# Kernel optimization log

Hardware: AMD Instinct MI355X
Metric: run time of the kernel (lower is better)

The kernel has to match this reference:

```python
import jax, jax.numpy as jnp
import numpy as np

GRID_SIZE = 5
SPLINE_ORDER = 3
HIDDEN = 128
N = 131072
K = 256          # num_cluster
EPS = 1e-8       # torch.cosine_similarity eps
N_COEF = GRID_SIZE + SPLINE_ORDER  # 8 spline basis functions per input feature


def make_grid():
    # efficient-kan grid: grid_range [-1,1], extended by spline_order on each side
    h = 2.0 / GRID_SIZE
    g = jnp.arange(-SPLINE_ORDER, GRID_SIZE + SPLINE_ORDER + 1, dtype=jnp.float32) * h - 1.0
    return jnp.tile(g[None, :], (HIDDEN, 1))  # (in, grid_size + 2*order + 1) = (128, 12)


def b_splines(x, grid):
    # x: (N, in), grid: (in, G) -> bases: (N, in, grid_size + spline_order)
    xe = x[..., None]
    bases = ((xe >= grid[:, :-1]) & (xe < grid[:, 1:])).astype(x.dtype)
    for p in range(1, SPLINE_ORDER + 1):
        left = (xe - grid[:, :-(p + 1)]) / (grid[:, p:-1] - grid[:, :-(p + 1)])
        right = (grid[:, p + 1:] - xe) / (grid[:, p + 1:] - grid[:, 1:-p])
        bases = left * bases[..., :-1] + right * bases[..., 1:]
    return bases


def kan_linear(x, grid, base_w, spline_w, scaler):
    # efficient-kan KANLinear: base path + spline path
    base = jax.nn.silu(x) @ base_w.T                       # (N, out)
    sp = b_splines(x, grid)                                # (N, in, coef)
    sw = spline_w * scaler[..., None]                      # (out, in, coef)
    return base + jnp.einsum('nic,oic->no', sp, sw)


def setup_inputs() -> dict:
    key = jax.random.key(0)
    ks = jax.random.split(key, 9)
    s = 1.0 / np.sqrt(HIDDEN)
    return {
        'x': jax.random.normal(ks[0], (N, HIDDEN), jnp.float32),
        'prototypes': jax.random.normal(ks[1], (K, HIDDEN), jnp.float32),
        'grid': make_grid(),
        'base_w1': jax.random.normal(ks[2], (HIDDEN, HIDDEN), jnp.float32) * s,
        'spline_w1': jax.random.normal(ks[3], (HIDDEN, HIDDEN, N_COEF), jnp.float32) * 0.1,
        'scaler1': jax.random.normal(ks[4], (HIDDEN, HIDDEN), jnp.float32) * s + 1.0,
        'base_w2': jax.random.normal(ks[5], (HIDDEN, HIDDEN), jnp.float32) * s,
        'spline_w2': jax.random.normal(ks[6], (HIDDEN, HIDDEN, N_COEF), jnp.float32) * 0.1,
        'scaler2': jax.random.normal(ks[7], (HIDDEN, HIDDEN), jnp.float32) * s + 1.0,
    }


def reference(x, prototypes, grid, base_w1, spline_w1, scaler1, base_w2, spline_w2, scaler2):
    # KAN([128,128,128]) = two KANLinear layers
    h = kan_linear(x, grid, base_w1, spline_w1, scaler1)
    emb = kan_linear(h, grid, base_w2, spline_w2, scaler2)     # (N, 128)
    # cosine similarity to all prototypes = normalized matmul (same math as
    # the broadcasted torch.cosine_similarity, without the (N,K,H) intermediate)
    xn = emb / jnp.maximum(jnp.linalg.norm(emb, axis=-1, keepdims=True), EPS)
    pn = prototypes / jnp.maximum(jnp.linalg.norm(prototypes, axis=-1, keepdims=True), EPS)
    sim = xn @ pn.T                                            # (N, K)
    cluster_assignments = jnp.argmax(sim, axis=1)              # (N,)
    return emb, cluster_assignments
```

## Files before the change

kernel.cpp:

```cpp
#include <hip/hip_runtime.h>
#include <math.h>

typedef unsigned short u16;
typedef _Float16 f16;
typedef __attribute__((ext_vector_type(8))) _Float16 f16x8;
typedef __attribute__((ext_vector_type(4))) float f32x4;

#define N_ROWS 131072
#define HID 128
#define WS_CH 8192
#define N_WCH 72
#define N_PCH 8

__device__ __forceinline__ void f16_split(float v, f16& hi, f16& lo) {
    f16 h = (f16)v;
    hi = h;
    lo = (f16)(v - (float)h);
}

__device__ __forceinline__ void spline8(float xv, float* a8) {
    float s  = (xv + 2.2f) * 2.5f;
    float tf = floorf(s);
    int   tt = (int)tf;
    bool valid = (tt >= 0) && (tt <= 10);
    float kt = (float)(tt - 3) * 0.4f - 1.0f;
    float u  = (xv - kt) * 2.5f;
    float u2 = u * u, u3 = u2 * u;
    float om = 1.0f - u;
    float b3 = u3 * (1.0f / 6.0f);
    float b2 = (-3.f * u3 + 3.f * u2 + 3.f * u + 1.f) * (1.0f / 6.0f);
    float b1 = (3.f * u3 - 6.f * u2 + 4.f) * (1.0f / 6.0f);
    float b0 = om * om * om * (1.0f / 6.0f);
    #pragma unroll
    for (int c = 0; c < 8; ++c) {
        int d = tt - c;
        float v = 0.f;
        v = (d == 0) ? b3 : v;
        v = (d == 1) ? b2 : v;
        v = (d == 2) ? b1 : v;
        v = (d == 3) ? b0 : v;
        a8[c] = valid ? v : 0.f;
    }
}

#define GLOAD_LDS16(g, l)                                                         \
    __builtin_amdgcn_global_load_lds(                                             \
        (const __attribute__((address_space(1))) unsigned int*)(g),               \
        (__attribute__((address_space(3))) unsigned int*)(l), 16, 0, 0)

__global__ __launch_bounds__(256)
void pack_weights(const float* __restrict__ bw1, const float* __restrict__ sw1,
                  const float* __restrict__ sc1,
                  const float* __restrict__ bw2, const float* __restrict__ sw2,
                  const float* __restrict__ sc2,
                  const float* __restrict__ protos, u16* __restrict__ ws)
{
    int gid = blockIdx.x * 256 + threadIdx.x;
    if (gid < N_WCH * 4096) {
        int l  = gid / (36 * 4096);
        int r  = gid % (36 * 4096);
        int ch = r / 4096;
        int e  = r % 4096;
        int o  = e >> 5;
        int kl = e & 31;
        const float* bw = l ? bw2 : bw1;
        const float* sw = l ? sw2 : sw1;
        const float* sc = l ? sc2 : sc1;
        float v;
        if (ch < 4) {
            v = bw[o * HID + ch * 32 + kl];
        } else {
            int i = (ch - 4) * 4 + (kl >> 3);
            v = sw[(o * HID + i) * 8 + (kl & 7)] * sc[o * HID + i];
        }
        f16 hi, lo; f16_split(v, hi, lo);
        int nt = o >> 4, n = o & 15, kq = kl >> 3, c = kl & 7;
        size_t base = (size_t)(l * 36 + ch) * WS_CH;
        size_t idx  = ((size_t)nt * 64 + kq * 16 + n) * 8 + c;
        ws[base + idx]        = __builtin_bit_cast(u16, hi);
        ws[base + 4096 + idx] = __builtin_bit_cast(u16, lo);
    } else if (gid < (N_WCH + N_PCH) * 4096) {
        int r  = gid - N_WCH * 4096;
        int hk = r / 4096;
        int e  = r % 4096;
        int pl = e >> 5;
        int kl = e & 31;
        int half = hk >> 2, kc = hk & 3;
        float v = protos[(size_t)(half * 128 + pl) * HID + kc * 32 + kl];
        f16 hi, lo; f16_split(v, hi, lo);
        int nt = pl >> 4, n = pl & 15, kq = kl >> 3, c = kl & 7;
        size_t base = (size_t)(N_WCH + hk) * WS_CH;
        size_t idx  = ((size_t)nt * 64 + kq * 16 + n) * 8 + c;
        ws[base + idx]        = __builtin_bit_cast(u16, hi);
        ws[base + 4096 + idx] = __builtin_bit_cast(u16, lo);
    }
}

__global__ __launch_bounds__(256, 3)
void kan_fused(const float* __restrict__ x, const float* __restrict__ protos,
               const u16* __restrict__ wpack,
               float* __restrict__ emb_out, float* __restrict__ assign_out)
{
    __shared__ float t[64][132];
    __shared__ u16   Bfrag[2][8][64][8];
    __shared__ float rnp[256];

    const int tid  = threadIdx.x;
    const int lane = tid & 63;
    const int w    = tid >> 6;
    const int m    = lane & 15;
    const int q    = lane >> 4;
    const int row  = w * 16 + m;
    const int brow = blockIdx.x * 64;

    {
        const float4* pr = (const float4*)(protos + (size_t)tid * HID);
        float s = 0.0f;
        #pragma unroll
        for (int j = 0; j < 32; ++j) {
            float4 v = pr[j];
            s += v.x * v.x + v.y * v.y + v.z * v.z + v.w * v.w;
        }
        rnp[tid] = 1.0f / fmaxf(sqrtf(s), 1e-8f);
    }

    {
        const int m2 = tid >> 2, kq2 = tid & 3;
        const float4* src = (const float4*)(x + (size_t)(brow + m2) * HID + kq2 * 32);
        #pragma unroll
        for (int j = 0; j < 8; ++j) {
            float4 v = src[j];
            int k = kq2 * 32 + j * 4;
            t[m2][k] = v.x; t[m2][k + 1] = v.y; t[m2][k + 2] = v.z; t[m2][k + 3] = v.w;
        }
    }
    __syncthreads();

    union { f16x8 v; f16 h[8]; } ah, al, bh, bl;
    f32x4 acc[8];

    for (int l = 0; l < 2; ++l) {
        #pragma unroll
        for (int nt = 0; nt < 8; ++nt) acc[nt] = (f32x4){0.f, 0.f, 0.f, 0.f};

        for (int ch = 0; ch < 36; ++ch) {
            float a8[8];
            if (ch < 4) {
                #pragma unroll
                for (int j = 0; j < 8; ++j) {
                    float xv = t[row][ch * 32 + q * 8 + j];
                    a8[j] = xv / (1.0f + expf(-xv));
                }
            } else {
                spline8(t[row][(ch - 4) * 4 + q], a8);
            }
            #pragma unroll
            for (int j = 0; j < 8; ++j) f16_split(a8[j], ah.h[j], al.h[j]);

            __syncthreads();
            {
                const char* gsrc = (const char*)(wpack + (size_t)(l * 36 + ch) * WS_CH);
                char* lbase = (char*)&Bfrag[0][0][0][0] + w * 4096;
                #pragma unroll
                for (int i = 0; i < 4; ++i)
                    GLOAD_LDS16(gsrc + w * 4096 + i * 1024 + (size_t)lane * 16,
                                lbase + i * 1024);
            }
            __syncthreads();

            #pragma unroll
            for (int nt = 0; nt < 8; ++nt) {
                bh.v = *(const f16x8*)Bfrag[0][nt][lane];
                bl.v = *(const f16x8*)Bfrag[1][nt][lane];
                acc[nt] = __builtin_amdgcn_mfma_f32_16x16x32_f16(ah.v, bh.v, acc[nt], 0, 0, 0);
                acc[nt] = __builtin_amdgcn_mfma_f32_16x16x32_f16(ah.v, bl.v, acc[nt], 0, 0, 0);
                acc[nt] = __builtin_amdgcn_mfma_f32_16x16x32_f16(al.v, bh.v, acc[nt], 0, 0, 0);
                acc[nt] = __builtin_amdgcn_mfma_f32_16x16x32_f16(al.v, bl.v, acc[nt], 0, 0, 0);
            }
        }

        #pragma unroll
        for (int nt = 0; nt < 8; ++nt)
            #pragma unroll
            for (int r = 0; r < 4; ++r)
                t[w * 16 + q * 4 + r][nt * 16 + m] = acc[nt][r];
        __syncthreads();
    }

    {
        const int m2 = tid >> 2, kq2 = tid & 3;
        float* dst = emb_out + (size_t)(brow + m2) * HID + kq2 * 32;
        #pragma unroll
        for (int j = 0; j < 8; ++j)
            *(float4*)(dst + j * 4) = *(const float4*)&t[m2][kq2 * 32 + j * 4];
    }

    float best[4]; int bi[4];
    #pragma unroll
    for (int r = 0; r < 4; ++r) { best[r] = -3.402823466e+38f; bi[r] = 0; }

    for (int half = 0; half < 2; ++half) {
        #pragma unroll
        for (int nt = 0; nt < 8; ++nt) acc[nt] = (f32x4){0.f, 0.f, 0.f, 0.f};

        for (int kc = 0; kc < 4; ++kc) {
            float a8[8];
            #pragma unroll
            for (int j = 0; j < 8; ++j) a8[j] = t[row][kc * 32 + q * 8 + j];
            #pragma unroll
            for (int j = 0; j < 8; ++j) f16_split(a8[j], ah.h[j], al.h[j]);

            __syncthreads();
            {
                const char* gsrc =
                    (const char*)(wpack + (size_t)(N_WCH + half * 4 + kc) * WS_CH);
                char* lbase = (char*)&Bfrag[0][0][0][0] + w * 4096;
                #pragma unroll
                for (int i = 0; i < 4; ++i)
                    GLOAD_LDS16(gsrc + w * 4096 + i * 1024 + (size_t)lane * 16,
                                lbase + i * 1024);
            }
            __syncthreads();

            #pragma unroll
            for (int nt = 0; nt < 8; ++nt) {
                bh.v = *(const f16x8*)Bfrag[0][nt][lane];
                bl.v = *(const f16x8*)Bfrag[1][nt][lane];
                acc[nt] = __builtin_amdgcn_mfma_f32_16x16x32_f16(ah.v, bh.v, acc[nt], 0, 0, 0);
                acc[nt] = __builtin_amdgcn_mfma_f32_16x16x32_f16(ah.v, bl.v, acc[nt], 0, 0, 0);
                acc[nt] = __builtin_amdgcn_mfma_f32_16x16x32_f16(al.v, bh.v, acc[nt], 0, 0, 0);
                acc[nt] = __builtin_amdgcn_mfma_f32_16x16x32_f16(al.v, bl.v, acc[nt], 0, 0, 0);
            }
        }

        #pragma unroll
        for (int nt = 0; nt < 8; ++nt) {
            int p = half * 128 + nt * 16 + m;
            float rp = rnp[p];
            #pragma unroll
            for (int r = 0; r < 4; ++r) {
                float v = acc[nt][r] * rp;
                if (v > best[r]) { best[r] = v; bi[r] = p; }
            }
        }
    }

    #pragma unroll
    for (int r = 0; r < 4; ++r) {
        #pragma unroll
        for (int off = 1; off < 16; off <<= 1) {
            float ov = __shfl_xor(best[r], off);
            int   oi = __shfl_xor(bi[r], off);
            if (ov > best[r] || (ov == best[r] && oi < bi[r])) { best[r] = ov; bi[r] = oi; }
        }
        if (m == 0)
            assign_out[(size_t)brow + w * 16 + q * 4 + r] = (float)bi[r];
    }
}

extern "C" void kernel_launch(void* const* d_in, const int* in_sizes, int n_in,
                              void* d_out, int out_size, void* d_ws, size_t ws_size,
                              hipStream_t stream) {
    (void)in_sizes; (void)n_in; (void)out_size; (void)ws_size;

    const float* x      = (const float*)d_in[0];
    const float* protos = (const float*)d_in[1];
    const float* bw1 = (const float*)d_in[3];
    const float* sw1 = (const float*)d_in[4];
    const float* sc1 = (const float*)d_in[5];
    const float* bw2 = (const float*)d_in[6];
    const float* sw2 = (const float*)d_in[7];
    const float* sc2 = (const float*)d_in[8];

    float* out    = (float*)d_out;
    float* embp   = out;
    float* assign = out + (size_t)N_ROWS * HID;
    u16*   wpack  = (u16*)d_ws;

    pack_weights<<<dim3((N_WCH + N_PCH) * 4096 / 256), dim3(256), 0, stream>>>(
        bw1, sw1, sc1, bw2, sw2, sc2, protos, wpack);
    kan_fused<<<dim3(N_ROWS / 64), dim3(256), 0, stream>>>(
        x, protos, wpack, embp, assign);
}
```

Baseline: 455.7 us.

## Register-prefetch weight chunks, drop lo*lo MFMA term, use fast SiLU

Weight loading moves from direct global-to-LDS loads to a register prefetch: the next chunk is issued into registers while the current chunk's MFMAs run, then stored to LDS after a barrier. This hides global load latency behind compute. The split-f16 product also drops the lo*lo MFMA, going from four to three per tile. SiLU now uses fast exp and rcp with vectorized LDS reads. These changes cut MFMA work and stall time at the cost of slightly lower precision and more registers held for the prefetch.

Result: faster. 425.1 us (-6.7%).

```diff
diff --git a/kernel.cpp b/kernel.cpp
--- a/kernel.cpp
+++ b/kernel.cpp
@@ -42,11 +42,6 @@
         a8[c] = valid ? v : 0.f;
     }
 }
-
-#define GLOAD_LDS16(g, l)                                                         \
-    __builtin_amdgcn_global_load_lds(                                             \
-        (const __attribute__((address_space(1))) unsigned int*)(g),               \
-        (__attribute__((address_space(3))) unsigned int*)(l), 16, 0, 0)
 
 __global__ __launch_bounds__(256)
 void pack_weights(const float* __restrict__ bw1, const float* __restrict__ sw1,
@@ -112,6 +107,27 @@
     const int q    = lane >> 4;
     const int row  = w * 16 + m;
     const int brow = blockIdx.x * 64;
+    const int woff = w * 256 + lane;
+
+    uint4 rr0, rr1, rr2, rr3;
+
+#define ISSUE_LOADS(region) do {                                                   \
+        const uint4* _g = (const uint4*)(wpack + (size_t)(region) * WS_CH) + woff; \
+        rr0 = _g[0]; rr1 = _g[64]; rr2 = _g[128]; rr3 = _g[192];                   \
+    } while (0)
+
+#define STORE_LDS() do {                                                           \
+        uint4* _l = (uint4*)&Bfrag[0][0][0][0] + woff;                             \
+        _l[0] = rr0; _l[64] = rr1; _l[128] = rr2; _l[192] = rr3;                   \
+    } while (0)
+
+#define PIPE_BARRIER() do {                                                        \
+        asm volatile("s_waitcnt lgkmcnt(0)" ::: "memory");                         \
+        __builtin_amdgcn_s_barrier();                                              \
+        __builtin_amdgcn_sched_barrier(0);                                         \
+    } while (0)
+
+    ISSUE_LOADS(0);
 
     {
         const float4* pr = (const float4*)(protos + (size_t)tid * HID);
@@ -134,7 +150,7 @@
             t[m2][k] = v.x; t[m2][k + 1] = v.y; t[m2][k + 2] = v.z; t[m2][k + 3] = v.w;
         }
     }
-    __syncthreads();
+    PIPE_BARRIER();
 
     union { f16x8 v; f16 h[8]; } ah, al, bh, bl;
     f32x4 acc[8];
@@ -146,36 +162,30 @@
         for (int ch = 0; ch < 36; ++ch) {
             float a8[8];
             if (ch < 4) {
+                const float4* tr = (const float4*)&t[row][ch * 32 + q * 8];
+                float4 v0 = tr[0], v1 = tr[1];
+                float xs[8] = {v0.x, v0.y, v0.z, v0.w, v1.x, v1.y, v1.z, v1.w};
                 #pragma unroll
-                for (int j = 0; j < 8; ++j) {
-                    float xv = t[row][ch * 32 + q * 8 + j];
-                    a8[j] = xv / (1.0f + expf(-xv));
-                }
+                for (int j = 0; j < 8; ++j)
+                    a8[j] = xs[j] * __builtin_amdgcn_rcpf(1.0f + __expf(-xs[j]));
             } else {
                 spline8(t[row][(ch - 4) * 4 + q], a8);
             }
             #pragma unroll
             for (int j = 0; j < 8; ++j) f16_split(a8[j], ah.h[j], al.h[j]);
 
-            __syncthreads();
-            {
-                const char* gsrc = (const char*)(wpack + (size_t)(l * 36 + ch) * WS_CH);
-                char* lbase = (char*)&Bfrag[0][0][0][0] + w * 4096;
-                #pragma unroll
-                for (int i = 0; i < 4; ++i)
-                    GLOAD_LDS16(gsrc + w * 4096 + i * 1024 + (size_t)lane * 16,
-                                lbase + i * 1024);
-            }
-            __syncthreads();
+            PIPE_BARRIER();
+            STORE_LDS();
+            ISSUE_LOADS(l * 36 + ch + 1);
+            PIPE_BARRIER();
 
             #pragma unroll
             for (int nt = 0; nt < 8; ++nt) {
                 bh.v = *(const f16x8*)Bfrag[0][nt][lane];
                 bl.v = *(const f16x8*)Bfrag[1][nt][lane];
                 acc[nt] = __builtin_amdgcn_mfma_f32_16x16x32_f16(ah.v, bh.v, acc[nt], 0, 0, 0);
+                acc[nt] = __builtin_amdgcn_mfma_f32_16x16x32_f16(al.v, bh.v, acc[nt], 0, 0, 0);
                 acc[nt] = __builtin_amdgcn_mfma_f32_16x16x32_f16(ah.v, bl.v, acc[nt], 0, 0, 0);
-                acc[nt] = __builtin_amdgcn_mfma_f32_16x16x32_f16(al.v, bh.v, acc[nt], 0, 0, 0);
-                acc[nt] = __builtin_amdgcn_mfma_f32_16x16x32_f16(al.v, bl.v, acc[nt], 0, 0, 0);
             }
         }
 
@@ -184,8 +194,9 @@
             #pragma unroll
             for (int r = 0; r < 4; ++r)
                 t[w * 16 + q * 4 + r][nt * 16 + m] = acc[nt][r];
-        __syncthreads();
-    }
+    }
+
+    PIPE_BARRIER();
 
     {
         const int m2 = tid >> 2, kq2 = tid & 3;
@@ -205,31 +216,30 @@
 
         for (int kc = 0; kc < 4; ++kc) {
             float a8[8];
-            #pragma unroll
-            for (int j = 0; j < 8; ++j) a8[j] = t[row][kc * 32 + q * 8 + j];
+            {
+                const float4* tr = (const float4*)&t[row][kc * 32 + q * 8];
+                float4 v0 = tr[0], v1 = tr[1];
+                a8[0] = v0.x; a8[1] = v0.y; a8[2] = v0.z; a8[3] = v0.w;
+                a8[4] = v1.x; a8[5] = v1.y; a8[6] = v1.z; a8[7] = v1.w;
+            }
             #pragma unroll
             for (int j = 0; j < 8; ++j) f16_split(a8[j], ah.h[j], al.h[j]);
 
-            __syncthreads();
+            PIPE_BARRIER();
+            STORE_LDS();
             {
-                const char* gsrc =
-                    (const char*)(wpack + (size_t)(N_WCH + half * 4 + kc) * WS_CH);
-                char* lbase = (char*)&Bfrag[0][0][0][0] + w * 4096;
-                #pragma unroll
-                for (int i = 0; i < 4; ++i)
-                    GLOAD_LDS16(gsrc + w * 4096 + i * 1024 + (size_t)lane * 16,
-                                lbase + i * 1024);
-            }
-            __syncthreads();
+                int nxt = 72 + half * 4 + kc + 1;
+                ISSUE_LOADS(nxt > 79 ? 79 : nxt);
+            }
+            PIPE_BARRIER();
 
             #pragma unroll
             for (int nt = 0; nt < 8; ++nt) {
                 bh.v = *(const f16x8*)Bfrag[0][nt][lane];
                 bl.v = *(const f16x8*)Bfrag[1][nt][lane];
                 acc[nt] = __builtin_amdgcn_mfma_f32_16x16x32_f16(ah.v, bh.v, acc[nt], 0, 0, 0);
+                acc[nt] = __builtin_amdgcn_mfma_f32_16x16x32_f16(al.v, bh.v, acc[nt], 0, 0, 0);
                 acc[nt] = __builtin_amdgcn_mfma_f32_16x16x32_f16(ah.v, bl.v, acc[nt], 0, 0, 0);
-                acc[nt] = __builtin_amdgcn_mfma_f32_16x16x32_f16(al.v, bh.v, acc[nt], 0, 0, 0);
-                acc[nt] = __builtin_amdgcn_mfma_f32_16x16x32_f16(al.v, bl.v, acc[nt], 0, 0, 0);
             }
         }
 
```
